# Kernel tuning notes

Measured on AMD Instinct MI355X. Metric: run time of the kernel, lower is better.

The kernel has to match this reference:

```python
import jax, jax.numpy as jnp
import numpy as np

N_HEADS = 16
DIM = 1024
DH = DIM // N_HEADS  # 64
B, S = 4, 2048


def setup_inputs() -> dict:
    key = jax.random.key(0)
    k1, k2, k3, k4 = jax.random.split(key, 4)
    x = jax.random.normal(k1, (B, S, DIM), dtype=jnp.float32)
    src_mask = jax.random.uniform(k2, (B, S)) < 0.1
    # torch nn.Linear weights: y = x @ W.T
    W_qkv = jax.random.normal(k3, (3 * DIM, DIM), dtype=jnp.float32) * (DIM ** -0.5)
    W_o = jax.random.normal(k4, (DIM, DIM), dtype=jnp.float32) * (DIM ** -0.5)
    return {"x": x, "src_mask": src_mask, "W_qkv": W_qkv, "W_o": W_o}


def reference(x, src_mask, W_qkv, W_o):
    b, s, _ = x.shape
    qkv = x @ W_qkv.T  # [b, s, 3*DIM]
    # rearrange 'b s (n_h d) -> ... ' BEFORE chunk(3): head h owns a contiguous
    # 3*DH slice, which is then split into q,k,v of DH each.
    qkv = qkv.reshape(b, s, N_HEADS, 3 * DH)
    q, k, v = jnp.split(qkv, 3, axis=-1)  # each [b, s, h, dh]
    logits = jnp.einsum('bqhd,bkhd->bhqk', q, k) * (DH ** -0.5)
    logits = jnp.where(src_mask[:, None, None, :], -jnp.inf, logits)
    attn = jax.nn.softmax(logits, axis=-1)  # dropout=0.0 -> identity
    out = jnp.einsum('bhqk,bkhd->bqhd', attn, v).reshape(b, s, DIM)
    return out @ W_o.T
```

## Files before the change

### kernel.cpp

```cpp
#include <hip/hip_runtime.h>
#include <hip/hip_bf16.h>
#include <stdint.h>


typedef unsigned short u16;
typedef __attribute__((ext_vector_type(8)))  short    bf16x8;
typedef __attribute__((ext_vector_type(8)))  unsigned short u16x8;
typedef __attribute__((ext_vector_type(4)))  unsigned short u16x4;
typedef __attribute__((ext_vector_type(4)))  float    f32x4;
typedef __attribute__((ext_vector_type(16))) float    f32x16;
typedef __attribute__((ext_vector_type(4)))  unsigned int u32x4;
typedef __attribute__((ext_vector_type(4)))  int      i32x4;

#define DEVI __device__ __forceinline__

DEVI u16 f2bf(float f) {
    union { float f; uint32_t u; } v; v.f = f;
    uint32_t r = v.u + 0x7fffu + ((v.u >> 16) & 1u);
    return (u16)(r >> 16);
}

DEVI float fexp2(float x) {
    float t = x + 12582912.0f;
    float f = x - (t - 12582912.0f);
    float p = 1.0f + f * (0.69314718f + f * (0.24022650f
                   + f * (0.05550411f + f * 0.00961813f)));
    uint32_t pb = __builtin_bit_cast(uint32_t, p)
                + (__builtin_bit_cast(uint32_t, t) << 23);
    return __builtin_bit_cast(float, pb);
}

#define GLDS(gp, lp) __builtin_amdgcn_global_load_lds( \
    (const __attribute__((address_space(1))) void*)(gp), \
    (__attribute__((address_space(3))) void*)(lp), 16, 0, 0)

#define MFMA16(a, b, c) __builtin_amdgcn_mfma_f32_16x16x32_bf16(a, b, c, 0, 0, 0)
#define MFMA32(a, b, c) __builtin_amdgcn_mfma_f32_32x32x16_bf16(a, b, c, 0, 0, 0)

#define CVTPK(d, lo, hi) asm("v_cvt_pk_bf16_f32 %0, %1, %2" : "=v"(d) : "v"(lo), "v"(hi))
#define PLSWAP(a, b) asm("v_permlane32_swap_b32 %0, %1" : "+v"(a), "+v"(b))

#define QSCALE 0.1803368801111204f

__global__ __launch_bounds__(256) void cvt_f32_bf16(const float* __restrict__ in,
                                                    u16* __restrict__ out, int n4) {
    int i = blockIdx.x * 256 + threadIdx.x;
    if (i >= n4) return;
    f32x4 v = *(const f32x4*)(in + (size_t)i * 4);
    u16x4 o;
#pragma unroll
    for (int j = 0; j < 4; j++) o[j] = f2bf(v[j]);
    *(u16x4*)(out + (size_t)i * 4) = o;
}

template <int MODE>
__global__ __launch_bounds__(256) void gemm_bt(const u16* __restrict__ A,
                                               const u16* __restrict__ B,
                                               void* __restrict__ C,
                                               int M, int N, int K) {
    __shared__ u16 As[128 * 32];
    __shared__ u16 Bs[128 * 32];
    const int lane = threadIdx.x & 63;
    const int wave = threadIdx.x >> 6;
    const int mT = blockIdx.y * 128;
    const int nT = blockIdx.x * 128;

    const int srow = wave * 16 + (lane >> 2);
    const int skc  = (lane & 3) * 8;
    const u16* gA = A + (size_t)(mT + srow) * K + skc;
    const u16* gB = B + (size_t)(nT + srow) * K + skc;
    u16* lA = As + wave * 512;
    u16* lB = Bs + wave * 512;

    f32x4 acc[4][4];
#pragma unroll
    for (int m = 0; m < 4; m++)
#pragma unroll
        for (int n = 0; n < 4; n++) acc[m][n] = f32x4{0.f, 0.f, 0.f, 0.f};

    const int wm = (wave >> 1) * 64, wn = (wave & 1) * 64;
    const int fr = lane & 15, fg = lane >> 4;

    for (int kt = 0; kt < K; kt += 32) {
        GLDS(gA + kt, lA);
        GLDS(gA + kt + (size_t)64 * K, lA + 2048);
        GLDS(gB + kt, lB);
        GLDS(gB + kt + (size_t)64 * K, lB + 2048);
        __syncthreads();
        bf16x8 af[4], bg[4];
#pragma unroll
        for (int m = 0; m < 4; m++)
            af[m] = *(const bf16x8*)(As + (wm + m * 16 + fr) * 32 + fg * 8);
#pragma unroll
        for (int n = 0; n < 4; n++)
            bg[n] = *(const bf16x8*)(Bs + (wn + n * 16 + fr) * 32 + fg * 8);
#pragma unroll
        for (int m = 0; m < 4; m++)
#pragma unroll
            for (int n = 0; n < 4; n++)
                acc[m][n] = MFMA16(af[m], bg[n], acc[m][n]);
        __syncthreads();
    }

    float qs[4];
#pragma unroll
    for (int n = 0; n < 4; n++) {
        if (MODE == 2) {
            int col = nT + wn + n * 16 + fr;
            qs[n] = ((col % 192) < 64) ? QSCALE : 1.0f;
        } else qs[n] = 1.0f;
    }
#pragma unroll
    for (int m = 0; m < 4; m++)
#pragma unroll
        for (int r = 0; r < 4; r++) {
            int row = mT + wm + m * 16 + fg * 4 + r;
#pragma unroll
            for (int n = 0; n < 4; n++) {
                int col = nT + wn + n * 16 + fr;
                if (MODE == 0) ((float*)C)[(size_t)row * N + col] = acc[m][n][r];
                else           ((u16*)C)[(size_t)row * N + col] = f2bf(acc[m][n][r] * qs[n]);
            }
        }
}

__global__ __launch_bounds__(256) void transpose_v(const u16* __restrict__ qkv,
                                                   const int* __restrict__ mask,
                                                   u16* __restrict__ vT) {
    __shared__ u16 tile[64][72];
    const int tid = threadIdx.x;
    const int b = blockIdx.z, h = blockIdx.y;
    const int s0 = blockIdx.x * 64;
    const int r = tid >> 3, c = tid & 7;

#pragma unroll
    for (int p = 0; p < 2; p++) {
        int s = p * 32 + r;
        u16x8 v = *(const u16x8*)(qkv + (size_t)(b * 2048 + s0 + s) * 3072
                                  + h * 192 + 128 + c * 8);
        if (mask[b * 2048 + s0 + s]) v = u16x8{0, 0, 0, 0, 0, 0, 0, 0};
#pragma unroll
        for (int j = 0; j < 8; j++) tile[c * 8 + j][s] = v[j];
    }
    __syncthreads();
#pragma unroll
    for (int p = 0; p < 2; p++) {
        int d = p * 32 + r;
        u16x8 v = *(const u16x8*)(&tile[d][c * 8]);
        *(u16x8*)(vT + ((size_t)((b * 16 + h) * 64 + d)) * 2048 + s0 + c * 8) = v;
    }
}

__global__ __launch_bounds__(256, 3) void attn_kernel(const u16* __restrict__ qkv,
                                                      const u16* __restrict__ vT,
                                                      const int* __restrict__ mask,
                                                      u16* __restrict__ ctx) {
    __shared__ u16 Kl[2][4096];
    __shared__ u16 Vl[2][4096];
    __shared__ u16 keeps[2048];

    const int lane = threadIdx.x & 63;
    const int wave = threadIdx.x >> 6;
    const int hl = lane >> 5;
    const int l31 = lane & 31;

    const int fid = blockIdx.x + 16 * blockIdx.y + 256 * blockIdx.z;
    const int swz = (fid & 7) * 128 + (fid >> 3);
    const int b = swz >> 8, h = (swz >> 4) & 15;
    const int qT = (swz & 15) * 128;

    {
        const i32x4* mp = (const i32x4*)(mask + b * 2048) + threadIdx.x * 2;
        i32x4 m0 = mp[0], m1 = mp[1];
        u16x8 kp;
#pragma unroll
        for (int j = 0; j < 4; j++) {
            kp[j]     = m0[j] ? (u16)0 : (u16)0x3F80;
            kp[4 + j] = m1[j] ? (u16)0 : (u16)0x3F80;
        }
        *(u16x8*)(keeps + threadIdx.x * 8) = kp;
    }

    const u16* qrow = qkv + (size_t)(b * 2048 + qT + wave * 32 + l31) * 3072 + h * 192;
    bf16x8 aq[4];
#pragma unroll
    for (int c = 0; c < 4; c++) aq[c] = *(const bf16x8*)(qrow + c * 16 + hl * 8);

    const int r0 = wave * 16 + (lane >> 3);
    const int j0 = (lane & 7) ^ (r0 & 7);
    const u16* kg = qkv + (size_t)(b * 2048 + r0) * 3072 + h * 192 + 64 + j0 * 8;
    const u16* vg = vT + ((size_t)((b * 16 + h) * 64) + r0) * 2048 + j0 * 8;

    u16* const lK0 = Kl[0] + wave * 1024;
    u16* const lV0 = Vl[0] + wave * 1024;
    u16* const lK1 = Kl[1] + wave * 1024;
    u16* const lV1 = Vl[1] + wave * 1024;

    {
        GLDS(kg, lK0); GLDS(kg + (size_t)8 * 3072, lK0 + 512);
        GLDS(vg, lV0); GLDS(vg + (size_t)8 * 2048, lV0 + 512);
    }

    const u16* kgn = kg + (size_t)64 * 3072;
    const u16* vgn = vg + 64;
    const u16* kpb = keeps + hl * 8;

    f32x16 so0, so1, lacc;
#pragma unroll
    for (int i = 0; i < 16; i++) { so0[i] = 0.f; so1[i] = 0.f; lacc[i] = 0.f; }
    f32x16 Z16;
#pragma unroll
    for (int i = 0; i < 16; i++) Z16[i] = 0.f;

    const int swc = l31 & 7;

    __syncthreads();

    int buf = 0;
    for (int t = 0; t < 32; ++t) {
        if (t < 31) {
            u16* lK = buf ? lK0 : lK1;
            u16* lV = buf ? lV0 : lV1;
            GLDS(kgn, lK); GLDS(kgn + (size_t)8 * 3072, lK + 512);
            GLDS(vgn, lV); GLDS(vgn + (size_t)8 * 2048, lV + 512);
            kgn += (size_t)64 * 3072;
            vgn += 64;
        }
        const u16* kc = Kl[buf];
        const u16* vc = Vl[buf];

        f32x16 s0, s1;
#pragma unroll
        for (int c = 0; c < 4; c++) {
            const int ch = ((c * 2 + hl) ^ swc) * 8;
            bf16x8 ka0 = *(const bf16x8*)(kc + l31 * 64 + ch);
            bf16x8 ka1 = *(const bf16x8*)(kc + (32 + l31) * 64 + ch);
            if (c == 0) {
                s0 = MFMA32(ka0, aq[0], Z16);
                s1 = MFMA32(ka1, aq[0], Z16);
            } else {
                s0 = MFMA32(ka0, aq[c], s0);
                s1 = MFMA32(ka1, aq[c], s1);
            }
        }

#pragma unroll
        for (int i = 0; i < 16; i++) { s0[i] = fexp2(s0[i]); s1[i] = fexp2(s1[i]); }

        uint32_t u0, u1, u2, u3, u4, u5, u6, u7;
        bf16x8 pa0, pa1, pa2, pa3;
        CVTPK(u0, s0[0], s0[1]);  CVTPK(u1, s0[2], s0[3]);
        CVTPK(u2, s0[4], s0[5]);  CVTPK(u3, s0[6], s0[7]);
        CVTPK(u4, s0[8], s0[9]);  CVTPK(u5, s0[10], s0[11]);
        CVTPK(u6, s0[12], s0[13]); CVTPK(u7, s0[14], s0[15]);
        PLSWAP(u0, u2); PLSWAP(u1, u3); PLSWAP(u4, u6); PLSWAP(u5, u7);
        pa0 = __builtin_bit_cast(bf16x8, u32x4{u0, u1, u2, u3});
        pa1 = __builtin_bit_cast(bf16x8, u32x4{u4, u5, u6, u7});
        CVTPK(u0, s1[0], s1[1]);  CVTPK(u1, s1[2], s1[3]);
        CVTPK(u2, s1[4], s1[5]);  CVTPK(u3, s1[6], s1[7]);
        CVTPK(u4, s1[8], s1[9]);  CVTPK(u5, s1[10], s1[11]);
        CVTPK(u6, s1[12], s1[13]); CVTPK(u7, s1[14], s1[15]);
        PLSWAP(u0, u2); PLSWAP(u1, u3); PLSWAP(u4, u6); PLSWAP(u5, u7);
        pa2 = __builtin_bit_cast(bf16x8, u32x4{u0, u1, u2, u3});
        pa3 = __builtin_bit_cast(bf16x8, u32x4{u4, u5, u6, u7});

#pragma unroll
        for (int c = 0; c < 4; c++) {
            const bf16x8 pa = (c == 0) ? pa0 : (c == 1) ? pa1 : (c == 2) ? pa2 : pa3;
            const int ch = ((c * 2 + hl) ^ swc) * 8;
            bf16x8 bv0 = *(const bf16x8*)(vc + l31 * 64 + ch);
            bf16x8 bv1 = *(const bf16x8*)(vc + (32 + l31) * 64 + ch);
            bf16x8 kp  = *(const bf16x8*)(kpb + c * 16);
            so0 = MFMA32(pa, bv0, so0);
            so1 = MFMA32(pa, bv1, so1);
            lacc = MFMA32(pa, kp, lacc);
        }
        kpb += 64;

        __syncthreads();
        buf ^= 1;
    }

#pragma unroll
    for (int r = 0; r < 16; r++) {
        const int q = qT + wave * 32 + (r & 3) + 8 * (r >> 2) + 4 * hl;
        const float inv = 1.0f / lacc[r];
        u16* crow = ctx + (size_t)(b * 2048 + q) * 1024 + h * 64 + l31;
        crow[0]  = f2bf(so0[r] * inv);
        crow[32] = f2bf(so1[r] * inv);
    }
}

extern "C" void kernel_launch(void* const* d_in, const int* in_sizes, int n_in,
                              void* d_out, int out_size, void* d_ws, size_t ws_size,
                              hipStream_t stream) {
    const float* x    = (const float*)d_in[0];
    const int*   mask = (const int*)d_in[1];
    const float* Wqkv = (const float*)d_in[2];
    const float* Wo   = (const float*)d_in[3];
    float* out = (float*)d_out;

    char* ws = (char*)d_ws;
    u16* xb    = (u16*)(ws);
    u16* wqkvb = (u16*)(ws + 16777216);
    u16* wob   = (u16*)(ws + 23068672);
    u16* qkvb  = (u16*)(ws + 25165824);
    u16* ctxb  = (u16*)(ws + 75497472);
    u16* vTb   = xb;

    cvt_f32_bf16<<<8192, 256, 0, stream>>>(x, xb, 8388608 / 4);
    cvt_f32_bf16<<<3072, 256, 0, stream>>>(Wqkv, wqkvb, 3145728 / 4);
    cvt_f32_bf16<<<1024, 256, 0, stream>>>(Wo, wob, 1048576 / 4);

    gemm_bt<2><<<dim3(24, 64), 256, 0, stream>>>(xb, wqkvb, qkvb, 8192, 3072, 1024);
    transpose_v<<<dim3(32, 16, 4), 256, 0, stream>>>(qkvb, mask, vTb);
    attn_kernel<<<dim3(16, 16, 4), 256, 0, stream>>>(qkvb, vTb, mask, ctxb);
    gemm_bt<0><<<dim3(8, 64), 256, 0, stream>>>(ctxb, wob, out, 8192, 1024, 1024);
}
```

Before: 238.3 us.

## Rewrite GEMMs with 256x128 tiles, double-buffered LDS, swizzle, and fused conversion

Replaces the 128x128 single-buffered GEMM with a 512-thread kernel that uses 256x128 tiles and a K-step of 64. Global loads into LDS are double-buffered so they overlap the MFMA work, the LDS layout is XOR-swizzled to avoid bank conflicts, and blocks are remapped so neighbouring blocks share operand tiles in L2. The three f32-to-bf16 conversion launches are merged into one kernel. The new GEMM hardcodes K=1024 (16 iterations), and its larger LDS footprint (96 KB) allows only one block per CU.

Measured after the change: 227.5 us. 1.05x faster.

```diff
diff --git a/kernel.cpp b/kernel.cpp
--- a/kernel.cpp
+++ b/kernel.cpp
@@ -42,81 +42,132 @@
 
 #define QSCALE 0.1803368801111204f
 
-__global__ __launch_bounds__(256) void cvt_f32_bf16(const float* __restrict__ in,
-                                                    u16* __restrict__ out, int n4) {
+__global__ __launch_bounds__(256) void cvt_all(const float* __restrict__ x,
+                                               const float* __restrict__ wqkv,
+                                               const float* __restrict__ wo,
+                                               u16* __restrict__ xb,
+                                               u16* __restrict__ wqkvb,
+                                               u16* __restrict__ wob) {
     int i = blockIdx.x * 256 + threadIdx.x;
-    if (i >= n4) return;
-    f32x4 v = *(const f32x4*)(in + (size_t)i * 4);
+    const float* src; u16* dst; int off;
+    if (i < 2097152)      { src = x;    dst = xb;    off = i; }
+    else if (i < 2883584) { src = wqkv; dst = wqkvb; off = i - 2097152; }
+    else                  { src = wo;   dst = wob;   off = i - 2883584; }
+    f32x4 v = *(const f32x4*)(src + (size_t)off * 4);
     u16x4 o;
 #pragma unroll
     for (int j = 0; j < 4; j++) o[j] = f2bf(v[j]);
-    *(u16x4*)(out + (size_t)i * 4) = o;
+    *(u16x4*)(dst + (size_t)off * 4) = o;
 }
 
 template <int MODE>
-__global__ __launch_bounds__(256) void gemm_bt(const u16* __restrict__ A,
-                                               const u16* __restrict__ B,
-                                               void* __restrict__ C,
-                                               int M, int N, int K) {
-    __shared__ u16 As[128 * 32];
-    __shared__ u16 Bs[128 * 32];
+__global__ __launch_bounds__(512, 1) void gemm_bt2(const u16* __restrict__ A,
+                                                   const u16* __restrict__ B,
+                                                   void* __restrict__ C,
+                                                   int M, int N, int K, int NT) {
+    __shared__ u16 Al[2][256 * 64];
+    __shared__ u16 Bl[2][128 * 64];
     const int lane = threadIdx.x & 63;
     const int wave = threadIdx.x >> 6;
-    const int mT = blockIdx.y * 128;
-    const int nT = blockIdx.x * 128;
-
-    const int srow = wave * 16 + (lane >> 2);
-    const int skc  = (lane & 3) * 8;
-    const u16* gA = A + (size_t)(mT + srow) * K + skc;
-    const u16* gB = B + (size_t)(nT + srow) * K + skc;
-    u16* lA = As + wave * 512;
-    u16* lB = Bs + wave * 512;
-
-    f32x4 acc[4][4];
-#pragma unroll
-    for (int m = 0; m < 4; m++)
-#pragma unroll
-        for (int n = 0; n < 4; n++) acc[m][n] = f32x4{0.f, 0.f, 0.f, 0.f};
-
-    const int wm = (wave >> 1) * 64, wn = (wave & 1) * 64;
+
+    const int fid = blockIdx.x;
+    const int swz = (fid & 7) * (gridDim.x >> 3) + (fid >> 3);
+    const int mT = (swz / NT) * 256;
+    const int nT = (swz % NT) * 128;
+
     const int fr = lane & 15, fg = lane >> 4;
-
-    for (int kt = 0; kt < K; kt += 32) {
-        GLDS(gA + kt, lA);
-        GLDS(gA + kt + (size_t)64 * K, lA + 2048);
-        GLDS(gB + kt, lB);
-        GLDS(gB + kt + (size_t)64 * K, lB + 2048);
-        __syncthreads();
-        bf16x8 af[4], bg[4];
-#pragma unroll
-        for (int m = 0; m < 4; m++)
-            af[m] = *(const bf16x8*)(As + (wm + m * 16 + fr) * 32 + fg * 8);
-#pragma unroll
-        for (int n = 0; n < 4; n++)
-            bg[n] = *(const bf16x8*)(Bs + (wn + n * 16 + fr) * 32 + fg * 8);
-#pragma unroll
-        for (int m = 0; m < 4; m++)
-#pragma unroll
-            for (int n = 0; n < 4; n++)
-                acc[m][n] = MFMA16(af[m], bg[n], acc[m][n]);
-        __syncthreads();
-    }
-
-    float qs[4];
-#pragma unroll
-    for (int n = 0; n < 4; n++) {
+    const int wm = (wave >> 2) * 128;
+    const int wn = (wave & 3) * 32;
+    const int sw = fr & 7;
+
+    const int sr = lane >> 3, sc = lane & 7;
+    const u16* gA = A + (size_t)(mT + wave * 32 + sr) * K + ((sc ^ sr) * 8);
+    const u16* gB = B + (size_t)(nT + wave * 16 + sr) * K + ((sc ^ sr) * 8);
+    u16* const dA0 = Al[0] + wave * 2048 + lane * 8;
+    u16* const dB0 = Bl[0] + wave * 1024 + lane * 8;
+    u16* const dA1 = Al[1] + wave * 2048 + lane * 8;
+    u16* const dB1 = Bl[1] + wave * 1024 + lane * 8;
+
+#define STG(t, dA, dB) do { \
+        const u16* pA = gA + (size_t)(t) * 64; \
+        const u16* pB = gB + (size_t)(t) * 64; \
+        GLDS(pA, dA);                  GLDS(pA + (size_t)8 * K, dA + 512); \
+        GLDS(pA + (size_t)16 * K, dA + 1024); GLDS(pA + (size_t)24 * K, dA + 1536); \
+        GLDS(pB, dB);                  GLDS(pB + (size_t)8 * K, dB + 512); \
+    } while (0)
+
+    f32x4 acc[8][2];
+#pragma unroll
+    for (int m = 0; m < 8; m++)
+#pragma unroll
+        for (int n = 0; n < 2; n++) acc[m][n] = f32x4{0.f, 0.f, 0.f, 0.f};
+
+    STG(0, dA0, dB0);
+    STG(1, dA1, dB1);
+
+    const int aoff = (wm + fr) * 64;
+    const int boff = (wn + fr) * 64;
+    const int ch0 = (fg ^ sw) * 8;
+    const int ch1 = ((4 + fg) ^ sw) * 8;
+
+    asm volatile("s_waitcnt vmcnt(6)" ::: "memory");
+    __builtin_amdgcn_s_barrier();
+
+    for (int t = 0; t < 16; ++t) {
+        const u16* al = Al[t & 1];
+        const u16* bl = Bl[t & 1];
+
+        __builtin_amdgcn_s_setprio(1);
+        {
+            bf16x8 b0 = *(const bf16x8*)(bl + boff + ch0);
+            bf16x8 b1 = *(const bf16x8*)(bl + boff + 1024 + ch0);
+#pragma unroll
+            for (int m = 0; m < 8; m++) {
+                bf16x8 a = *(const bf16x8*)(al + aoff + m * 1024 + ch0);
+                acc[m][0] = MFMA16(a, b0, acc[m][0]);
+                acc[m][1] = MFMA16(a, b1, acc[m][1]);
+            }
+        }
+        {
+            bf16x8 b2 = *(const bf16x8*)(bl + boff + ch1);
+            bf16x8 b3 = *(const bf16x8*)(bl + boff + 1024 + ch1);
+#pragma unroll
+            for (int m = 0; m < 8; m++) {
+                bf16x8 a = *(const bf16x8*)(al + aoff + m * 1024 + ch1);
+                acc[m][0] = MFMA16(a, b2, acc[m][0]);
+                acc[m][1] = MFMA16(a, b3, acc[m][1]);
+            }
+        }
+        __builtin_amdgcn_s_setprio(0);
+
+        __builtin_amdgcn_s_barrier();
+        if (t < 14) {
+            if (t & 1) STG(t + 2, dA1, dB1);
+            else       STG(t + 2, dA0, dB0);
+        }
+        if (t < 15) {
+            if (t < 14) asm volatile("s_waitcnt vmcnt(6)" ::: "memory");
+            else        asm volatile("s_waitcnt vmcnt(0)" ::: "memory");
+            __builtin_amdgcn_s_barrier();
+        }
+    }
+#undef STG
+
+    float qs[2];
+#pragma unroll
+    for (int n = 0; n < 2; n++) {
         if (MODE == 2) {
             int col = nT + wn + n * 16 + fr;
             qs[n] = ((col % 192) < 64) ? QSCALE : 1.0f;
         } else qs[n] = 1.0f;
     }
 #pragma unroll
-    for (int m = 0; m < 4; m++)
+    for (int m = 0; m < 8; m++)
 #pragma unroll
         for (int r = 0; r < 4; r++) {
             int row = mT + wm + m * 16 + fg * 4 + r;
 #pragma unroll
-            for (int n = 0; n < 4; n++) {
+            for (int n = 0; n < 2; n++) {
                 int col = nT + wn + n * 16 + fr;
                 if (MODE == 0) ((float*)C)[(size_t)row * N + col] = acc[m][n][r];
                 else           ((u16*)C)[(size_t)row * N + col] = f2bf(acc[m][n][r] * qs[n]);
@@ -308,12 +359,10 @@
     u16* ctxb  = (u16*)(ws + 75497472);
     u16* vTb   = xb;
 
-    cvt_f32_bf16<<<8192, 256, 0, stream>>>(x, xb, 8388608 / 4);
-    cvt_f32_bf16<<<3072, 256, 0, stream>>>(Wqkv, wqkvb, 3145728 / 4);
-    cvt_f32_bf16<<<1024, 256, 0, stream>>>(Wo, wob, 1048576 / 4);
-
-    gemm_bt<2><<<dim3(24, 64), 256, 0, stream>>>(xb, wqkvb, qkvb, 8192, 3072, 1024);
+    cvt_all<<<12288, 256, 0, stream>>>(x, Wqkv, Wo, xb, wqkvb, wob);
+
+    gemm_bt2<2><<<768, 512, 0, stream>>>(xb, wqkvb, qkvb, 8192, 3072, 1024, 24);
     transpose_v<<<dim3(32, 16, 4), 256, 0, stream>>>(qkvb, mask, vTb);
     attn_kernel<<<dim3(16, 16, 4), 256, 0, stream>>>(qkvb, vTb, mask, ctxb);
-    gemm_bt<0><<<dim3(8, 64), 256, 0, stream>>>(ctxb, wob, out, 8192, 1024, 1024);
-}
+    gemm_bt2<0><<<256, 512, 0, stream>>>(ctxb, wob, out, 8192, 1024, 1024, 8);
+}
```
